# Optimization experiments

Hardware: AMD Instinct MI355X
Metric: run time of the kernel (lower is better)

## Reference

```python
import jax, jax.numpy as jnp
import numpy as np

B, V, H, T, D, HD = 4, 384, 128, 16, 8, 64
N = V + H  # 512
relu = jax.nn.relu


def setup_inputs() -> dict:
    key = jax.random.key(0)
    ks = jax.random.split(key, 12)

    def w(k, i, o):
        return (jax.random.normal(k, (i, o), jnp.float32) / np.sqrt(i)).astype(jnp.float32)

    return {
        "x": jax.random.normal(ks[0], (B, V, T, D), jnp.float32),
        "adj": jax.random.uniform(ks[1], (B, N, N), jnp.float32),
        # input_proj: Linear(T*D, HD) -> ReLU -> Linear(HD, HD) -> ReLU
        "w_in1": w(ks[2], T * D, HD), "b_in1": jnp.zeros((HD,), jnp.float32),
        "w_in2": w(ks[3], HD, HD), "b_in2": jnp.zeros((HD,), jnp.float32),
        # edge_mlp: Linear(2*HD, HD) -> ReLU -> Linear(HD, HD) -> ReLU
        "w_e1": w(ks[4], 2 * HD, HD), "b_e1": jnp.zeros((HD,), jnp.float32),
        "w_e2": w(ks[5], HD, HD), "b_e2": jnp.zeros((HD,), jnp.float32),
        # node_mlp: Linear(HD, HD) -> ReLU -> Linear(HD, HD) -> ReLU
        "w_n1": w(ks[6], HD, HD), "b_n1": jnp.zeros((HD,), jnp.float32),
        "w_n2": w(ks[7], HD, HD), "b_n2": jnp.zeros((HD,), jnp.float32),
        # out_proj: Linear(HD, T*D)
        "w_out": w(ks[8], HD, T * D), "b_out": jnp.zeros((T * D,), jnp.float32),
    }


def reference(x, adj, w_in1, b_in1, w_in2, b_in2, w_e1, b_e1, w_e2, b_e2,
              w_n1, b_n1, w_n2, b_n2, w_out, b_out):
    # node embedding of visible nodes: (B,V,HD)
    h = relu(relu(x.reshape(B, V, T * D) @ w_in1 + b_in1) @ w_in2 + b_in2)
    # pad hidden nodes with zeros: (B,N,HD)
    h_full = jnp.zeros((B, N, HD), x.dtype).at[:, :V].set(h)
    # edge_mlp layer 1 on cat([h_i, h_j]): split weight instead of materializing
    # the (B,N,N,2*HD) concatenation — same math.
    a = h_full @ w_e1[:HD]   # receiver-side contribution (B,N,HD)
    b = h_full @ w_e1[HD:]   # sender-side contribution  (B,N,HD)
    e = relu(a[:, :, None, :] + b[:, None, :, :] + b_e1)   # (B,N,N,HD)
    e = relu(e @ w_e2 + b_e2)                               # (B,N,N,HD)
    # mask by adjacency and sum over senders j
    agg = jnp.einsum('bijh,bij->bih', e, adj)               # (B,N,HD)
    n = relu(relu(agg @ w_n1 + b_n1) @ w_n2 + b_n2)         # (B,N,HD)
    out = n[:, V:] @ w_out + b_out                          # (B,H,T*D)
    return out.reshape(B, H, T, D)
```

## Files before the change

### kernel.cpp

```cpp
#include <hip/hip_runtime.h>

#define BQ 4
#define VV 384
#define HH 128
#define NN 512
#define HDIM 64
#define TD 128

__device__ __forceinline__ float BCAST(float v, int l) {
    return __int_as_float(__builtin_amdgcn_readlane(__float_as_int(v), l));
}

__global__ __launch_bounds__(128) void k_rowpipe(
    const float* __restrict__ x,
    const float* __restrict__ w_in1,
    const float* __restrict__ b_in1,
    const float* __restrict__ w_in2,
    const float* __restrict__ b_in2,
    const float* __restrict__ w_e1,
    const float* __restrict__ b_e1,
    const float* __restrict__ w_e2,
    const float* __restrict__ b_e2,
    float* __restrict__ E2)
{
    __shared__ float part[2][HDIM];

    const int hf   = threadIdx.x >> 6;
    const int lane = threadIdx.x & 63;
    const int row  = blockIdx.x;

    const float* xr = x + (size_t)row * TD;
    const float xv = xr[64 * hf + lane];

    float a0 = 0.f, a1 = 0.f;
    #pragma unroll 8
    for (int k = 0; k < 64; k += 2) {
        const int kg = 64 * hf + k;
        a0 = fmaf(BCAST(xv, k),     w_in1[kg * HDIM + lane],       a0);
        a1 = fmaf(BCAST(xv, k + 1), w_in1[(kg + 1) * HDIM + lane], a1);
    }
    part[hf][lane] = a0 + a1;
    __syncthreads();
    const float h1 = fmaxf(part[0][lane] + part[1][lane] + b_in1[lane], 0.f);

    a0 = b_in2[lane]; a1 = 0.f;
    #pragma unroll 8
    for (int k = 0; k < HDIM; k += 2) {
        a0 = fmaf(BCAST(h1, k),     w_in2[k * HDIM + lane],       a0);
        a1 = fmaf(BCAST(h1, k + 1), w_in2[(k + 1) * HDIM + lane], a1);
    }
    const float h2 = fmaxf(a0 + a1, 0.f);

    a0 = 0.f; a1 = 0.f;
    #pragma unroll 8
    for (int k = 0; k < HDIM; k += 2) {
        a0 = fmaf(BCAST(h2, k),     w_e1[(HDIM + k) * HDIM + lane],     a0);
        a1 = fmaf(BCAST(h2, k + 1), w_e1[(HDIM + k + 1) * HDIM + lane], a1);
    }
    const float e1 = fmaxf(a0 + a1 + b_e1[lane], 0.f);

    a0 = b_e2[lane]; a1 = 0.f;
    #pragma unroll 8
    for (int k = 0; k < HDIM; k += 2) {
        a0 = fmaf(BCAST(e1, k),     w_e2[k * HDIM + lane],       a0);
        a1 = fmaf(BCAST(e1, k + 1), w_e2[(k + 1) * HDIM + lane], a1);
    }
    if (hf == 0)
        E2[(size_t)row * HDIM + lane] = fmaxf(a0 + a1, 0.f);
}

__global__ __launch_bounds__(1024) void k_agg_out(
    const float* __restrict__ adj,
    const float* __restrict__ E2,
    const float* __restrict__ b_e1, const float* __restrict__ w_e2,
    const float* __restrict__ b_e2,
    const float* __restrict__ w_n1, const float* __restrict__ b_n1,
    const float* __restrict__ w_n2, const float* __restrict__ b_n2,
    const float* __restrict__ w_out,
    const float* __restrict__ b_out,
    float* __restrict__ out)
{
    const int blk  = blockIdx.x;
    const int b    = blk >> 6;
    const int pair = blk & 63;
    const int wid  = threadIdx.x >> 6;
    const int lane = threadIdx.x & 63;

    const int i0 = VV + pair * 2;
    const float* adjr0 = adj + ((size_t)b * NN + i0) * NN;
    const float* adjr1 = adjr0 + NN;
    const int j0 = wid * 32;

    const float adjv = (lane < 32) ? adjr0[j0 + lane] : adjr1[j0 + lane - 32];

    __shared__ float redA[12][2][HDIM];
    __shared__ float hs[4][2];
    __shared__ float e2c[HDIM];

    if (wid < 12) {
        const float* e2b = E2 + ((size_t)b * VV + j0) * HDIM;
        float p0 = 0.f, p1 = 0.f, q0 = 0.f, q1 = 0.f;
        #pragma unroll 8
        for (int jj = 0; jj < 32; jj += 2) {
            const float e0 = e2b[jj * HDIM + lane];
            const float e1 = e2b[(jj + 1) * HDIM + lane];
            p0 = fmaf(BCAST(adjv, jj),      e0, p0);
            q0 = fmaf(BCAST(adjv, 32 + jj), e0, q0);
            p1 = fmaf(BCAST(adjv, jj + 1),  e1, p1);
            q1 = fmaf(BCAST(adjv, 33 + jj), e1, q1);
        }
        redA[wid][0][lane] = p0 + p1;
        redA[wid][1][lane] = q0 + q1;
    } else {
        float s = adjv;
        s += __shfl_xor(s, 1, 64);
        s += __shfl_xor(s, 2, 64);
        s += __shfl_xor(s, 4, 64);
        s += __shfl_xor(s, 8, 64);
        s += __shfl_xor(s, 16, 64);
        if (lane == 0)  hs[wid - 12][0] = s;
        if (lane == 32) hs[wid - 12][1] = s;
        if (wid == 12) {
            const float e1c = fmaxf(b_e1[lane], 0.f);
            float t0 = b_e2[lane], t1 = 0.f;
            #pragma unroll 8
            for (int k = 0; k < HDIM; k += 2) {
                t0 = fmaf(BCAST(e1c, k),     w_e2[k * HDIM + lane],       t0);
                t1 = fmaf(BCAST(e1c, k + 1), w_e2[(k + 1) * HDIM + lane], t1);
            }
            e2c[lane] = fmaxf(t0 + t1, 0.f);
        }
    }
    __syncthreads();

    const int g  = wid >> 3;
    const int w8 = wid & 7;

    const float hsum = hs[0][g] + hs[1][g] + hs[2][g] + hs[3][g];
    float agg = hsum * e2c[lane];
    #pragma unroll
    for (int w = 0; w < 12; ++w) agg += redA[w][g][lane];

    __shared__ float redB[16][HDIM];
    {
        float t0 = 0.f, t1 = 0.f;
        #pragma unroll
        for (int t = 0; t < 8; t += 2) {
            const int k = 8 * w8 + t;
            t0 = fmaf(BCAST(agg, k),     w_n1[k * HDIM + lane],       t0);
            t1 = fmaf(BCAST(agg, k + 1), w_n1[(k + 1) * HDIM + lane], t1);
        }
        redB[wid][lane] = t0 + t1;
    }
    __syncthreads();
    float n1 = b_n1[lane];
    #pragma unroll
    for (int w = 0; w < 8; ++w) n1 += redB[g * 8 + w][lane];
    n1 = fmaxf(n1, 0.f);

    __shared__ float redC[16][HDIM];
    {
        float t0 = 0.f, t1 = 0.f;
        #pragma unroll
        for (int t = 0; t < 8; t += 2) {
            const int k = 8 * w8 + t;
            t0 = fmaf(BCAST(n1, k),     w_n2[k * HDIM + lane],       t0);
            t1 = fmaf(BCAST(n1, k + 1), w_n2[(k + 1) * HDIM + lane], t1);
        }
        redC[wid][lane] = t0 + t1;
    }
    __syncthreads();
    float n2 = b_n2[lane];
    #pragma unroll
    for (int w = 0; w < 8; ++w) n2 += redC[g * 8 + w][lane];
    n2 = fmaxf(n2, 0.f);

    __shared__ float redD[16][TD];
    {
        float o0 = 0.f, o1 = 0.f;
        #pragma unroll
        for (int t = 0; t < 8; ++t) {
            const int k = 8 * w8 + t;
            const float v = BCAST(n2, k);
            o0 = fmaf(v, w_out[k * TD + lane],      o0);
            o1 = fmaf(v, w_out[k * TD + 64 + lane], o1);
        }
        redD[wid][lane]      = o0;
        redD[wid][64 + lane] = o1;
    }
    __syncthreads();

    if (w8 < 2) {
        const int col = w8 * 64 + lane;
        float o = b_out[col];
        #pragma unroll
        for (int w = 0; w < 8; ++w) o += redD[g * 8 + w][col];
        const int orow = b * HH + pair * 2 + g;
        out[(size_t)orow * TD + col] = o;
    }
}

extern "C" void kernel_launch(void* const* d_in, const int* in_sizes, int n_in,
                              void* d_out, int out_size, void* d_ws, size_t ws_size,
                              hipStream_t stream) {
    const float* x     = (const float*)d_in[0];
    const float* adj   = (const float*)d_in[1];
    const float* w_in1 = (const float*)d_in[2];
    const float* b_in1 = (const float*)d_in[3];
    const float* w_in2 = (const float*)d_in[4];
    const float* b_in2 = (const float*)d_in[5];
    const float* w_e1  = (const float*)d_in[6];
    const float* b_e1  = (const float*)d_in[7];
    const float* w_e2  = (const float*)d_in[8];
    const float* b_e2  = (const float*)d_in[9];
    const float* w_n1  = (const float*)d_in[10];
    const float* b_n1  = (const float*)d_in[11];
    const float* w_n2  = (const float*)d_in[12];
    const float* b_n2  = (const float*)d_in[13];
    const float* w_out = (const float*)d_in[14];
    const float* b_out = (const float*)d_in[15];
    float* out = (float*)d_out;
    float* E2  = (float*)d_ws;

    k_rowpipe<<<BQ * VV, 128, 0, stream>>>(
        x, w_in1, b_in1, w_in2, b_in2, w_e1, b_e1, w_e2, b_e2, E2);
    k_agg_out<<<BQ * HH / 2, 1024, 0, stream>>>(
        adj, E2, b_e1, w_e2, b_e2, w_n1, b_n1, w_n2, b_n2, w_out, b_out, out);
}
```

Before: 19.56 us.

## Process two rows per block with packed float2 math and K-split across four waves

```diff
diff --git a/kernel.cpp b/kernel.cpp
--- a/kernel.cpp
+++ b/kernel.cpp
@@ -7,11 +7,16 @@
 #define HDIM 64
 #define TD 128
 
+typedef float f32x2 __attribute__((ext_vector_type(2)));
+
 __device__ __forceinline__ float BCAST(float v, int l) {
     return __int_as_float(__builtin_amdgcn_readlane(__float_as_int(v), l));
 }
-
-__global__ __launch_bounds__(128) void k_rowpipe(
+__device__ __forceinline__ f32x2 RELU2(f32x2 v) {
+    f32x2 r; r.x = fmaxf(v.x, 0.f); r.y = fmaxf(v.y, 0.f); return r;
+}
+
+__global__ __launch_bounds__(256) void k_rowpipe(
     const float* __restrict__ x,
     const float* __restrict__ w_in1,
     const float* __restrict__ b_in1,
@@ -23,50 +28,82 @@
     const float* __restrict__ b_e2,
     float* __restrict__ E2)
 {
-    __shared__ float part[2][HDIM];
-
-    const int hf   = threadIdx.x >> 6;
+    __shared__ f32x2 part[4][4][HDIM];
+
+    const int q    = threadIdx.x >> 6;
     const int lane = threadIdx.x & 63;
-    const int row  = blockIdx.x;
-
-    const float* xr = x + (size_t)row * TD;
-    const float xv = xr[64 * hf + lane];
-
-    float a0 = 0.f, a1 = 0.f;
-    #pragma unroll 8
-    for (int k = 0; k < 64; k += 2) {
-        const int kg = 64 * hf + k;
-        a0 = fmaf(BCAST(xv, k),     w_in1[kg * HDIM + lane],       a0);
-        a1 = fmaf(BCAST(xv, k + 1), w_in1[(kg + 1) * HDIM + lane], a1);
-    }
-    part[hf][lane] = a0 + a1;
-    __syncthreads();
-    const float h1 = fmaxf(part[0][lane] + part[1][lane] + b_in1[lane], 0.f);
-
-    a0 = b_in2[lane]; a1 = 0.f;
-    #pragma unroll 8
-    for (int k = 0; k < HDIM; k += 2) {
-        a0 = fmaf(BCAST(h1, k),     w_in2[k * HDIM + lane],       a0);
-        a1 = fmaf(BCAST(h1, k + 1), w_in2[(k + 1) * HDIM + lane], a1);
-    }
-    const float h2 = fmaxf(a0 + a1, 0.f);
-
-    a0 = 0.f; a1 = 0.f;
-    #pragma unroll 8
-    for (int k = 0; k < HDIM; k += 2) {
-        a0 = fmaf(BCAST(h2, k),     w_e1[(HDIM + k) * HDIM + lane],     a0);
-        a1 = fmaf(BCAST(h2, k + 1), w_e1[(HDIM + k + 1) * HDIM + lane], a1);
-    }
-    const float e1 = fmaxf(a0 + a1 + b_e1[lane], 0.f);
-
-    a0 = b_e2[lane]; a1 = 0.f;
-    #pragma unroll 8
-    for (int k = 0; k < HDIM; k += 2) {
-        a0 = fmaf(BCAST(e1, k),     w_e2[k * HDIM + lane],       a0);
-        a1 = fmaf(BCAST(e1, k + 1), w_e2[(k + 1) * HDIM + lane], a1);
-    }
-    if (hf == 0)
-        E2[(size_t)row * HDIM + lane] = fmaxf(a0 + a1, 0.f);
+    const int row0 = blockIdx.x * 2;
+
+    const float* xr0 = x + (size_t)row0 * TD;
+    const float* xr1 = xr0 + TD;
+    const float xv = (lane < 32) ? xr0[32 * q + lane] : xr1[32 * q + lane - 32];
+
+    f32x2 a0 = {0.f, 0.f}, a1 = {0.f, 0.f};
+    #pragma unroll 8
+    for (int k = 0; k < 32; k += 2) {
+        const int kg = 32 * q + k;
+        f32x2 s0; s0.x = BCAST(xv, k);     s0.y = BCAST(xv, 32 + k);
+        f32x2 s1; s1.x = BCAST(xv, k + 1); s1.y = BCAST(xv, 33 + k);
+        a0 += s0 * w_in1[kg * HDIM + lane];
+        a1 += s1 * w_in1[(kg + 1) * HDIM + lane];
+    }
+    part[0][q][lane] = a0 + a1;
+    __syncthreads();
+    f32x2 t = (part[0][0][lane] + part[0][1][lane])
+            + (part[0][2][lane] + part[0][3][lane]);
+    const f32x2 h1 = RELU2(t + b_in1[lane]);
+    const float h1x = h1.x, h1y = h1.y;
+
+    a0 = (f32x2){0.f, 0.f}; a1 = (f32x2){0.f, 0.f};
+    #pragma unroll 8
+    for (int k = 0; k < 16; k += 2) {
+        const int kg = 16 * q + k;
+        f32x2 s0; s0.x = BCAST(h1x, kg);     s0.y = BCAST(h1y, kg);
+        f32x2 s1; s1.x = BCAST(h1x, kg + 1); s1.y = BCAST(h1y, kg + 1);
+        a0 += s0 * w_in2[kg * HDIM + lane];
+        a1 += s1 * w_in2[(kg + 1) * HDIM + lane];
+    }
+    part[1][q][lane] = a0 + a1;
+    __syncthreads();
+    t = (part[1][0][lane] + part[1][1][lane])
+      + (part[1][2][lane] + part[1][3][lane]);
+    const f32x2 h2 = RELU2(t + b_in2[lane]);
+    const float h2x = h2.x, h2y = h2.y;
+
+    a0 = (f32x2){0.f, 0.f}; a1 = (f32x2){0.f, 0.f};
+    #pragma unroll 8
+    for (int k = 0; k < 16; k += 2) {
+        const int kg = 16 * q + k;
+        f32x2 s0; s0.x = BCAST(h2x, kg);     s0.y = BCAST(h2y, kg);
+        f32x2 s1; s1.x = BCAST(h2x, kg + 1); s1.y = BCAST(h2y, kg + 1);
+        a0 += s0 * w_e1[(HDIM + kg) * HDIM + lane];
+        a1 += s1 * w_e1[(HDIM + kg + 1) * HDIM + lane];
+    }
+    part[2][q][lane] = a0 + a1;
+    __syncthreads();
+    t = (part[2][0][lane] + part[2][1][lane])
+      + (part[2][2][lane] + part[2][3][lane]);
+    const f32x2 e1 = RELU2(t + b_e1[lane]);
+    const float e1x = e1.x, e1y = e1.y;
+
+    a0 = (f32x2){0.f, 0.f}; a1 = (f32x2){0.f, 0.f};
+    #pragma unroll 8
+    for (int k = 0; k < 16; k += 2) {
+        const int kg = 16 * q + k;
+        f32x2 s0; s0.x = BCAST(e1x, kg);     s0.y = BCAST(e1y, kg);
+        f32x2 s1; s1.x = BCAST(e1x, kg + 1); s1.y = BCAST(e1y, kg + 1);
+        a0 += s0 * w_e2[kg * HDIM + lane];
+        a1 += s1 * w_e2[(kg + 1) * HDIM + lane];
+    }
+    part[3][q][lane] = a0 + a1;
+    __syncthreads();
+    if (q == 0) {
+        t = (part[3][0][lane] + part[3][1][lane])
+          + (part[3][2][lane] + part[3][3][lane]);
+        const f32x2 e2v = RELU2(t + b_e2[lane]);
+        E2[(size_t)row0 * HDIM + lane]       = e2v.x;
+        E2[(size_t)(row0 + 1) * HDIM + lane] = e2v.y;
+    }
 }
 
 __global__ __launch_bounds__(1024) void k_agg_out(
@@ -222,7 +259,7 @@
     float* out = (float*)d_out;
     float* E2  = (float*)d_ws;
 
-    k_rowpipe<<<BQ * VV, 128, 0, stream>>>(
+    k_rowpipe<<<BQ * VV / 2, 256, 0, stream>>>(
         x, w_in1, b_in1, w_in2, b_in2, w_e1, b_e1, w_e2, b_e2, E2);
     k_agg_out<<<BQ * HH / 2, 1024, 0, stream>>>(
         adj, E2, b_e1, w_e2, b_e2, w_n1, b_n1, w_n2, b_n2, w_out, b_out, out);
```

New measurement: 16.65 us. -14.9%, faster.
